# Performance work log

Measured on AMD Instinct MI355X. Metric: run time of the kernel, lower is better.

The kernel has to match this reference:

```python
import jax, jax.numpy as jnp
import numpy as np

HEADS = 8


def setup_inputs() -> dict:
    key = jax.random.key(0)
    ks = jax.random.split(key, 5)
    B, C, H, W = 2, 256, 48, 48
    s = 0.02
    return {
        "ct": jax.random.normal(ks[0], (B, C, H, W), jnp.float32),
        "us": jax.random.normal(ks[1], (B, C, H, W), jnp.float32),
        "w_qkv_ct": jax.random.normal(ks[2], (3 * C, C), jnp.float32) * s,
        "w_qkv_us": jax.random.normal(ks[3], (3 * C, C), jnp.float32) * s,
        "w_proj": jax.random.normal(ks[4], (C, 2 * C), jnp.float32) * s,
        "b_proj": jnp.zeros((C,), jnp.float32),
    }


def _heads_view(x, B, H, W):
    # [B, C, H, W] -> [B, heads, HW, dh]
    C = x.shape[1]
    return x.reshape(B, HEADS, C // HEADS, H * W).transpose(0, 1, 3, 2)


def _cross_attn(q, k, v, scale):
    # q,k,v: [B, heads, HW, dh]
    attn = jax.nn.softmax(jnp.einsum("bhnd,bhmd->bhnm", q, k) * scale, axis=-1)
    return jnp.einsum("bhnm,bhmd->bhnd", attn, v)


def reference(ct, us, w_qkv_ct, w_qkv_us, w_proj, b_proj):
    B, C, H, W = ct.shape
    dh = C // HEADS
    scale = dh ** (-0.5)

    # 1x1 convs as channel GEMMs
    qkv1 = jnp.einsum("oc,bchw->bohw", w_qkv_ct, ct)
    qkv2 = jnp.einsum("oc,bchw->bohw", w_qkv_us, us)
    q1, k1, v1 = jnp.split(qkv1, 3, axis=1)
    q2, k2, v2 = jnp.split(qkv2, 3, axis=1)

    # CT queries attend to US keys/values
    o1 = _cross_attn(_heads_view(q1, B, H, W), _heads_view(k2, B, H, W),
                     _heads_view(v2, B, H, W), scale)
    # US queries attend to CT keys/values
    o2 = _cross_attn(_heads_view(q2, B, H, W), _heads_view(k1, B, H, W),
                     _heads_view(v1, B, H, W), scale)

    # [B, heads, HW, dh] -> [B, C, H, W]
    out1 = o1.transpose(0, 1, 3, 2).reshape(B, C, H, W)
    out2 = o2.transpose(0, 1, 3, 2).reshape(B, C, H, W)

    fused = jnp.concatenate([ct + out1, us + out2], axis=1)
    return jnp.einsum("oc,bchw->bohw", w_proj, fused) + b_proj[None, :, None, None]
```

## Files before the change

### kernel.cpp

```cpp
#include <hip/hip_runtime.h>
#include <hip/hip_bf16.h>
#include <math.h>

#define HW   2304
#define CCH  256

#define QSCALE 0.25504368686637270f

typedef short short8 __attribute__((ext_vector_type(8)));
typedef float f32x4  __attribute__((ext_vector_type(4)));

__device__ inline unsigned short f2bf(float f) {
    union { float f; unsigned u; } v; v.f = f;
    unsigned r = v.u + 0x7FFF + ((v.u >> 16) & 1);
    return (unsigned short)(r >> 16);
}
__device__ inline unsigned pkbf2(float a, float b) {
    float2 f; f.x = a; f.y = b;
    union { __hip_bfloat162 h; unsigned u; } c;
    c.h = __float22bfloat162_rn(f);
    return c.u;
}
__device__ inline unsigned pktrunc(float a, float b) {
    return __builtin_amdgcn_perm(__builtin_bit_cast(unsigned, b),
                                 __builtin_bit_cast(unsigned, a), 0x07060302u);
}


__device__ __forceinline__ void prep_unit(
    int u, int t,
    const float* __restrict__ ct, const float* __restrict__ us,
    const float* __restrict__ w1, const float* __restrict__ w2,
    const float* __restrict__ w3,
    unsigned short* __restrict__ xT,
    unsigned short* __restrict__ wb1, unsigned short* __restrict__ wb2,
    unsigned short* __restrict__ w3b,
    unsigned short* __restrict__ Ts )
{
    if (u >= 576) {
        const int v_ = u - 576;
        int z, base;
        if (v_ < 192)      { z = 0; base = v_ * 1024; }
        else if (v_ < 384) { z = 1; base = (v_ - 192) * 1024; }
        else               { z = 2; base = (v_ - 384) * 1024; }
        const float* s = (z == 0) ? w1 : (z == 1) ? w2 : w3;
        unsigned short* d = (z == 0) ? wb1 : (z == 1) ? wb2 : w3b;
        const int i = base + t * 4;
        const float4 v4 = *(const float4*)&s[i];
        const float sc = (z < 2 && i < 65536) ? QSCALE : 1.f;
        uint2 p; p.x = pkbf2(v4.x * sc, v4.y * sc); p.y = pkbf2(v4.z * sc, v4.w * sc);
        *(uint2*)&d[i] = p;
        return;
    }
    const int pt = u % 36, rest = u / 36, ctile = rest & 3, z = rest >> 2;
    const float* __restrict__ src = ((z >> 1) ? us : ct) + (size_t)(z & 1) * CCH * HW;
    unsigned short* __restrict__ dst = xT + (size_t)z * HW * 256;
    const int p0 = pt * 64, c0 = ctile * 64;
    const int m = t & 15, ms = (m & 7) << 3;
    __syncthreads();
#pragma unroll
    for (int r = 0; r < 4; r++) {
        const int c = (t >> 4) + 16 * r;
        const float4 v4 = *(const float4*)&src[(size_t)(c0 + c) * HW + p0 + m * 4];
        const int cs = c ^ ms;
        Ts[(m * 4 + 0) * 72 + cs] = f2bf(v4.x);
        Ts[(m * 4 + 1) * 72 + cs] = f2bf(v4.y);
        Ts[(m * 4 + 2) * 72 + cs] = f2bf(v4.z);
        Ts[(m * 4 + 3) * 72 + cs] = f2bf(v4.w);
    }
    __syncthreads();
    const int p = t >> 2, c8 = (t & 3) * 16;
    const int es = ((p >> 2) & 7) << 3;
    const short8 a  = *(const short8*)&Ts[p * 72 + (c8 ^ es)];
    const short8 b8 = *(const short8*)&Ts[p * 72 + ((c8 + 8) ^ es)];
    *(short8*)&dst[(size_t)(p0 + p) * 256 + c0 + c8]     = a;
    *(short8*)&dst[(size_t)(p0 + p) * 256 + c0 + c8 + 8] = b8;
}

__device__ __forceinline__ void qkv_unit(
    int ptile, int otile, int z, int t,
    const unsigned short* __restrict__ xT,
    const unsigned short* __restrict__ wb1, const unsigned short* __restrict__ wb2,
    unsigned short* __restrict__ qkvT1, unsigned short* __restrict__ qkvT2,
    unsigned short* __restrict__ vdm1,  unsigned short* __restrict__ vdm2,
    unsigned short* __restrict__ Ws, unsigned short* __restrict__ Xs)
{
    const int inp = z >> 1, b = z & 1;
    const unsigned short* __restrict__ X = xT + (size_t)(inp * 2 + b) * HW * 256;
    const unsigned short* __restrict__ W = inp ? wb2 : wb1;
    unsigned short* __restrict__ qT = (inp ? qkvT2 : qkvT1) + (size_t)b * HW * 512;
    unsigned short* __restrict__ vd = (inp ? vdm2 : vdm1) + (size_t)b * CCH * HW;
    const int p0 = ptile * 64, o0 = otile * 64;
    const int w = t >> 6, lane = t & 63, quad = lane >> 4, m = lane & 15;
    const int sr = t >> 3, sc = t & 7;

    f32x4 acc[4] = {{0,0,0,0},{0,0,0,0},{0,0,0,0},{0,0,0,0}};

    short8 wv0 = *(const short8*)&W[(size_t)(o0 + sr) * 256 + sc * 8];
    short8 wv1 = *(const short8*)&W[(size_t)(o0 + 32 + sr) * 256 + sc * 8];
    short8 xv0 = *(const short8*)&X[(size_t)(p0 + sr) * 256 + sc * 8];
    short8 xv1 = *(const short8*)&X[(size_t)(p0 + 32 + sr) * 256 + sc * 8];

    for (int k0 = 0; k0 < 256; k0 += 64) {
        __syncthreads();
        *(short8*)&Ws[sr * 72 + sc * 8] = wv0;
        *(short8*)&Ws[(32 + sr) * 72 + sc * 8] = wv1;
        *(short8*)&Xs[sr * 72 + sc * 8] = xv0;
        *(short8*)&Xs[(32 + sr) * 72 + sc * 8] = xv1;
        __syncthreads();
        const int kn = k0 + 64;
        if (kn < 256) {
            wv0 = *(const short8*)&W[(size_t)(o0 + sr) * 256 + kn + sc * 8];
            wv1 = *(const short8*)&W[(size_t)(o0 + 32 + sr) * 256 + kn + sc * 8];
            xv0 = *(const short8*)&X[(size_t)(p0 + sr) * 256 + kn + sc * 8];
            xv1 = *(const short8*)&X[(size_t)(p0 + 32 + sr) * 256 + kn + sc * 8];
        }
#pragma unroll
        for (int kc2 = 0; kc2 < 2; kc2++) {
            const short8 af = *(const short8*)&Ws[(w * 16 + m) * 72 + kc2 * 32 + quad * 8];
#pragma unroll
            for (int pg = 0; pg < 4; pg++) {
                const short8 bf = *(const short8*)&Xs[(pg * 16 + m) * 72 + kc2 * 32 + quad * 8];
                acc[pg] = __builtin_amdgcn_mfma_f32_16x16x32_bf16(af, bf, acc[pg], 0, 0, 0);
            }
        }
    }
    __syncthreads();
    if (o0 < 512) {
#pragma unroll
        for (int pg = 0; pg < 4; pg++) {
            uint2 pk; pk.x = pkbf2(acc[pg][0], acc[pg][1]); pk.y = pkbf2(acc[pg][2], acc[pg][3]);
            *(uint2*)&Ws[(pg * 16 + m) * 72 + w * 16 + quad * 4] = pk;
        }
        __syncthreads();
        const int pr = t >> 2, cc = t & 3;
        const uint4 d0 = *(const uint4*)&Ws[pr * 72 + cc * 16];
        const uint4 d1 = *(const uint4*)&Ws[pr * 72 + cc * 16 + 8];
        *(uint4*)&qT[(size_t)(p0 + pr) * 512 + o0 + cc * 16]     = d0;
        *(uint4*)&qT[(size_t)(p0 + pr) * 512 + o0 + cc * 16 + 8] = d1;
    } else {
#pragma unroll
        for (int pg = 0; pg < 4; pg++)
#pragma unroll
            for (int r = 0; r < 4; r++)
                Ws[(w * 16 + quad * 4 + r) * 72 + pg * 16 + m] = f2bf(acc[pg][r]);
        __syncthreads();
        const int dr = t >> 2, cc = t & 3;
        const uint4 d0 = *(const uint4*)&Ws[dr * 72 + cc * 16];
        const uint4 d1 = *(const uint4*)&Ws[dr * 72 + cc * 16 + 8];
        *(uint4*)&vd[(size_t)(o0 - 512 + dr) * HW + p0 + cc * 16]     = d0;
        *(uint4*)&vd[(size_t)(o0 - 512 + dr) * HW + p0 + cc * 16 + 8] = d1;
    }
    __syncthreads();
}

__device__ __forceinline__ void attn_unit(
    int ptile, int dir, int b, int h, int t,
    const unsigned short* __restrict__ qkvT1, const unsigned short* __restrict__ qkvT2,
    const unsigned short* __restrict__ vdm1,  const unsigned short* __restrict__ vdm2,
    const float* __restrict__ ct, const float* __restrict__ us,
    unsigned short* __restrict__ fusedT,
    unsigned short* __restrict__ Ks , unsigned short* __restrict__ Vs )
{
    const unsigned short* __restrict__ Qt = (dir ? qkvT2 : qkvT1) + (size_t)b * HW * 512;
    const unsigned short* __restrict__ Kt = (dir ? qkvT1 : qkvT2) + (size_t)b * HW * 512
                                            + 256 + h * 32;
    const unsigned short* __restrict__ Vd = (dir ? vdm1 : vdm2) + ((size_t)b * CCH + h * 32) * HW;
    const float* __restrict__ src = (dir ? us : ct) + ((size_t)b * CCH + h * 32) * HW;

    const int w = t >> 6, lane = t & 63, quad = lane >> 4, m = lane & 15;
    const int kj0 = t >> 2, kcs = t & 3;
    const int pcK = kcs ^ (((kj0 >> 1) & 1) | (((kj0 >> 3) & 1) << 1));
    const int vr0 = t >> 4, vcs = t & 15;
    const int g2m = ((m >> 1) & 1) | (((m >> 2) & 1) << 1);
    const unsigned short* __restrict__ ksb =
        &Ks[((m >> 2) * 8 + (m & 3)) * 32 + (quad ^ g2m) * 8];
    const unsigned short* __restrict__ vsb = &Vs[m * 136 + quad * 8];
    const short ONE = (short)0x3F80;
    const short8 ones = {ONE,ONE,ONE,ONE,ONE,ONE,ONE,ONE};

    const int pqA = ptile * 128 + w * 32 + m;
    const short8 qfA = *(const short8*)&Qt[(size_t)pqA * 512 + h * 32 + quad * 8];
    const short8 qfB = *(const short8*)&Qt[(size_t)(pqA + 16) * 512 + h * 32 + quad * 8];

    f32x4 acc0A = {0,0,0,0}, acc1A = {0,0,0,0}, acclA = {0,0,0,0};
    f32x4 acc0B = {0,0,0,0}, acc1B = {0,0,0,0}, acclB = {0,0,0,0};

    short8 ka = *(const short8*)&Kt[(size_t)kj0 * 512 + kcs * 8];
    short8 kb = *(const short8*)&Kt[(size_t)(kj0 + 64) * 512 + kcs * 8];
    short8 va = *(const short8*)&Vd[(size_t)vr0 * HW + vcs * 8];
    short8 vb = *(const short8*)&Vd[(size_t)(vr0 + 16) * HW + vcs * 8];

    for (int j0 = 0; j0 < HW; j0 += 128) {
        __syncthreads();
        *(short8*)&Ks[kj0 * 32 + pcK * 8] = ka;
        *(short8*)&Ks[(kj0 + 64) * 32 + pcK * 8] = kb;
        *(short8*)&Vs[vr0 * 136 + vcs * 8] = va;
        *(short8*)&Vs[(vr0 + 16) * 136 + vcs * 8] = vb;
        __syncthreads();

        const int jn = j0 + 128;
        if (jn < HW) {
            ka = *(const short8*)&Kt[(size_t)(jn + kj0) * 512 + kcs * 8];
            kb = *(const short8*)&Kt[(size_t)(jn + kj0 + 64) * 512 + kcs * 8];
            va = *(const short8*)&Vd[(size_t)vr0 * HW + jn + vcs * 8];
            vb = *(const short8*)&Vd[(size_t)(vr0 + 16) * HW + jn + vcs * 8];
        }

        uint4 pwA[4], pwB[4];
#pragma unroll
        for (int f = 0; f < 8; f++) {
            const short8 kf = *(const short8*)(ksb + ((f >> 1) * 32 + (f & 1) * 4) * 32);
            const f32x4 z = {0,0,0,0};
            const f32x4 SA = __builtin_amdgcn_mfma_f32_16x16x32_bf16(kf, qfA, z, 0, 0, 0);
            const f32x4 SB = __builtin_amdgcn_mfma_f32_16x16x32_bf16(kf, qfB, z, 0, 0, 0);
            const float a0 = __builtin_amdgcn_exp2f(SA[0]);
            const float a1 = __builtin_amdgcn_exp2f(SA[1]);
            const float a2 = __builtin_amdgcn_exp2f(SA[2]);
            const float a3 = __builtin_amdgcn_exp2f(SA[3]);
            const float b0 = __builtin_amdgcn_exp2f(SB[0]);
            const float b1 = __builtin_amdgcn_exp2f(SB[1]);
            const float b2 = __builtin_amdgcn_exp2f(SB[2]);
            const float b3 = __builtin_amdgcn_exp2f(SB[3]);
            if ((f & 1) == 0) {
                pwA[f >> 1].x = pktrunc(a0, a1); pwA[f >> 1].y = pktrunc(a2, a3);
                pwB[f >> 1].x = pktrunc(b0, b1); pwB[f >> 1].y = pktrunc(b2, b3);
            } else {
                pwA[f >> 1].z = pktrunc(a0, a1); pwA[f >> 1].w = pktrunc(a2, a3);
                pwB[f >> 1].z = pktrunc(b0, b1); pwB[f >> 1].w = pktrunc(b2, b3);
            }
        }
#pragma unroll
        for (int kt = 0; kt < 4; kt++) {
            const short8 pfA = __builtin_bit_cast(short8, pwA[kt]);
            const short8 pfB = __builtin_bit_cast(short8, pwB[kt]);
            const short8 vf0 = *(const short8*)(vsb + kt * 32);
            const short8 vf1 = *(const short8*)(vsb + 16 * 136 + kt * 32);
            acc0A = __builtin_amdgcn_mfma_f32_16x16x32_bf16(vf0, pfA, acc0A, 0, 0, 0);
            acc1A = __builtin_amdgcn_mfma_f32_16x16x32_bf16(vf1, pfA, acc1A, 0, 0, 0);
            acclA = __builtin_amdgcn_mfma_f32_16x16x32_bf16(ones, pfA, acclA, 0, 0, 0);
            acc0B = __builtin_amdgcn_mfma_f32_16x16x32_bf16(vf0, pfB, acc0B, 0, 0, 0);
            acc1B = __builtin_amdgcn_mfma_f32_16x16x32_bf16(vf1, pfB, acc1B, 0, 0, 0);
            acclB = __builtin_amdgcn_mfma_f32_16x16x32_bf16(ones, pfB, acclB, 0, 0, 0);
        }
    }

    const int cb = dir * 256 + h * 32, d0 = quad * 4;
    {
        const float inv = 1.f / acclA[0];
        unsigned short* __restrict__ fT = fusedT + ((size_t)b * HW + pqA) * 512 + cb + d0;
        uint2 s0, s1;
        s0.x = pkbf2(acc0A[0] * inv + src[(size_t)(d0 + 0) * HW + pqA],
                     acc0A[1] * inv + src[(size_t)(d0 + 1) * HW + pqA]);
        s0.y = pkbf2(acc0A[2] * inv + src[(size_t)(d0 + 2) * HW + pqA],
                     acc0A[3] * inv + src[(size_t)(d0 + 3) * HW + pqA]);
        s1.x = pkbf2(acc1A[0] * inv + src[(size_t)(16 + d0 + 0) * HW + pqA],
                     acc1A[1] * inv + src[(size_t)(16 + d0 + 1) * HW + pqA]);
        s1.y = pkbf2(acc1A[2] * inv + src[(size_t)(16 + d0 + 2) * HW + pqA],
                     acc1A[3] * inv + src[(size_t)(16 + d0 + 3) * HW + pqA]);
        *(uint2*)&fT[0]  = s0;
        *(uint2*)&fT[16] = s1;
    }
    {
        const int pqB = pqA + 16;
        const float inv = 1.f / acclB[0];
        unsigned short* __restrict__ fT = fusedT + ((size_t)b * HW + pqB) * 512 + cb + d0;
        uint2 s0, s1;
        s0.x = pkbf2(acc0B[0] * inv + src[(size_t)(d0 + 0) * HW + pqB],
                     acc0B[1] * inv + src[(size_t)(d0 + 1) * HW + pqB]);
        s0.y = pkbf2(acc0B[2] * inv + src[(size_t)(d0 + 2) * HW + pqB],
                     acc0B[3] * inv + src[(size_t)(d0 + 3) * HW + pqB]);
        s1.x = pkbf2(acc1B[0] * inv + src[(size_t)(16 + d0 + 0) * HW + pqB],
                     acc1B[1] * inv + src[(size_t)(16 + d0 + 1) * HW + pqB]);
        s1.y = pkbf2(acc1B[2] * inv + src[(size_t)(16 + d0 + 2) * HW + pqB],
                     acc1B[3] * inv + src[(size_t)(16 + d0 + 3) * HW + pqB]);
        *(uint2*)&fT[0]  = s0;
        *(uint2*)&fT[16] = s1;
    }
    __syncthreads();
}

__device__ __forceinline__ void proj_unit(
    int ptile, int otile, int t,
    const unsigned short* __restrict__ w3b, const unsigned short* __restrict__ fusedT,
    const float* __restrict__ bias, float* __restrict__ out,
    unsigned short* __restrict__ Ws, unsigned short* __restrict__ Xs)
{
    const int p0 = ptile * 64, o0 = otile * 64;
    const int w = t >> 6, lane = t & 63, quad = lane >> 4, m = lane & 15;
    const int sr = t >> 3, sc = t & 7;

    f32x4 acc[4] = {{0,0,0,0},{0,0,0,0},{0,0,0,0},{0,0,0,0}};

    short8 wv0 = *(const short8*)&w3b[(size_t)(o0 + sr) * 512 + sc * 8];
    short8 wv1 = *(const short8*)&w3b[(size_t)(o0 + 32 + sr) * 512 + sc * 8];
    short8 xv0 = *(const short8*)&fusedT[(size_t)(p0 + sr) * 512 + sc * 8];
    short8 xv1 = *(const short8*)&fusedT[(size_t)(p0 + 32 + sr) * 512 + sc * 8];

    for (int k0 = 0; k0 < 512; k0 += 64) {
        __syncthreads();
        *(short8*)&Ws[sr * 72 + sc * 8] = wv0;
        *(short8*)&Ws[(32 + sr) * 72 + sc * 8] = wv1;
        *(short8*)&Xs[sr * 72 + sc * 8] = xv0;
        *(short8*)&Xs[(32 + sr) * 72 + sc * 8] = xv1;
        __syncthreads();
        const int kn = k0 + 64;
        if (kn < 512) {
            wv0 = *(const short8*)&w3b[(size_t)(o0 + sr) * 512 + kn + sc * 8];
            wv1 = *(const short8*)&w3b[(size_t)(o0 + 32 + sr) * 512 + kn + sc * 8];
            xv0 = *(const short8*)&fusedT[(size_t)(p0 + sr) * 512 + kn + sc * 8];
            xv1 = *(const short8*)&fusedT[(size_t)(p0 + 32 + sr) * 512 + kn + sc * 8];
        }
#pragma unroll
        for (int kc2 = 0; kc2 < 2; kc2++) {
            const short8 af = *(const short8*)&Ws[(w * 16 + m) * 72 + kc2 * 32 + quad * 8];
#pragma unroll
            for (int pg = 0; pg < 4; pg++) {
                const short8 bf = *(const short8*)&Xs[(pg * 16 + m) * 72 + kc2 * 32 + quad * 8];
                acc[pg] = __builtin_amdgcn_mfma_f32_16x16x32_bf16(af, bf, acc[pg], 0, 0, 0);
            }
        }
    }
    const int b = (p0 >= HW) ? 1 : 0;
    const int pl0 = p0 - b * HW;
    float* __restrict__ ob = out + (size_t)b * CCH * HW;
    float b4[4];
#pragma unroll
    for (int r = 0; r < 4; r++) b4[r] = bias[o0 + w * 16 + quad * 4 + r];
#pragma unroll
    for (int pg = 0; pg < 4; pg++)
#pragma unroll
        for (int r = 0; r < 4; r++)
            ob[(size_t)(o0 + w * 16 + quad * 4 + r) * HW + pl0 + pg * 16 + m]
                = acc[pg][r] + b4[r];
}

__global__ __launch_bounds__(256, 4) void prep_k(
    const float* __restrict__ ct, const float* __restrict__ us,
    const float* __restrict__ w1, const float* __restrict__ w2,
    const float* __restrict__ w3,
    unsigned short* __restrict__ xT,
    unsigned short* __restrict__ b1, unsigned short* __restrict__ b2,
    unsigned short* __restrict__ b3)
{
    __shared__ __align__(16) unsigned short Ts[64 * 72];
    prep_unit(blockIdx.x, threadIdx.x, ct, us, w1, w2, w3, xT, b1, b2, b3, Ts);
}

__global__ __launch_bounds__(256, 4) void qkv_k(
    const unsigned short* __restrict__ xT,
    const unsigned short* __restrict__ wb1, const unsigned short* __restrict__ wb2,
    unsigned short* __restrict__ qkvT1, unsigned short* __restrict__ qkvT2,
    unsigned short* __restrict__ vdm1,  unsigned short* __restrict__ vdm2)
{
    __shared__ __align__(16) unsigned short Ws[64 * 72];
    __shared__ __align__(16) unsigned short Xs[64 * 72];
    qkv_unit(blockIdx.x, blockIdx.y, blockIdx.z, threadIdx.x,
             xT, wb1, wb2, qkvT1, qkvT2, vdm1, vdm2, Ws, Xs);
}

__global__ __launch_bounds__(256, 3) void attn_k(
    const unsigned short* __restrict__ qkvT1, const unsigned short* __restrict__ qkvT2,
    const unsigned short* __restrict__ vdm1,  const unsigned short* __restrict__ vdm2,
    const float* __restrict__ ct, const float* __restrict__ us,
    unsigned short* __restrict__ fusedT)
{
    __shared__ __align__(16) unsigned short Ks[128 * 32];
    __shared__ __align__(16) unsigned short Vs[32 * 136];
    attn_unit(blockIdx.x, blockIdx.z, blockIdx.y >> 3, blockIdx.y & 7, threadIdx.x,
              qkvT1, qkvT2, vdm1, vdm2, ct, us, fusedT, Ks, Vs);
}

__global__ __launch_bounds__(256, 4) void proj_k(
    const unsigned short* __restrict__ w3b, const unsigned short* __restrict__ fusedT,
    const float* __restrict__ bias, float* __restrict__ out)
{
    __shared__ __align__(16) unsigned short Ws[64 * 72];
    __shared__ __align__(16) unsigned short Xs[64 * 72];
    proj_unit(blockIdx.x, blockIdx.y, threadIdx.x, w3b, fusedT, bias, out, Ws, Xs);
}

extern "C" void kernel_launch(void* const* d_in, const int* in_sizes, int n_in,
                              void* d_out, int out_size, void* d_ws, size_t ws_size,
                              hipStream_t stream)
{
    const float* ct       = (const float*)d_in[0];
    const float* us       = (const float*)d_in[1];
    const float* w_qkv_ct = (const float*)d_in[2];
    const float* w_qkv_us = (const float*)d_in[3];
    const float* w_proj   = (const float*)d_in[4];
    const float* b_proj   = (const float*)d_in[5];
    float* out = (float*)d_out;

    unsigned short* wb1   = (unsigned short*)d_ws;
    unsigned short* wb2   = wb1 + (size_t)768 * 256;
    unsigned short* w3b   = wb2 + (size_t)768 * 256;
    unsigned short* xT    = w3b + (size_t)256 * 512;
    unsigned short* qkvT1 = xT    + (size_t)4 * HW * 256;
    unsigned short* qkvT2 = qkvT1 + (size_t)2 * HW * 512;
    unsigned short* vdm1  = qkvT2 + (size_t)2 * HW * 512;
    unsigned short* vdm2  = vdm1  + (size_t)2 * CCH * HW;
    unsigned short* fusedT= vdm2  + (size_t)2 * CCH * HW;

    prep_k<<<dim3(1088), 256, 0, stream>>>(ct, us, w_qkv_ct, w_qkv_us, w_proj,
                                           xT, wb1, wb2, w3b);
    qkv_k <<<dim3(36, 12, 4), 256, 0, stream>>>(xT, wb1, wb2, qkvT1, qkvT2, vdm1, vdm2);
    attn_k<<<dim3(18, 16, 2), 256, 0, stream>>>(qkvT1, qkvT2, vdm1, vdm2, ct, us, fusedT);
    proj_k<<<dim3(72, 4), 256, 0, stream>>>(w3b, fusedT, b_proj, out);
}
```

Baseline: 125.4 us.

## Keep full X tile resident in LDS and loop over three output tiles per block

Result: slower. 128.0 us (+2.0%).

```diff
diff --git a/kernel.cpp b/kernel.cpp
--- a/kernel.cpp
+++ b/kernel.cpp
@@ -56,7 +56,7 @@
     const float* __restrict__ src = ((z >> 1) ? us : ct) + (size_t)(z & 1) * CCH * HW;
     unsigned short* __restrict__ dst = xT + (size_t)z * HW * 256;
     const int p0 = pt * 64, c0 = ctile * 64;
-    const int m = t & 15, ms = (m & 7) << 3;
+    const int m = t & 15, ms = ((m >> 1) & 7) << 3;
     __syncthreads();
 #pragma unroll
     for (int r = 0; r < 4; r++) {
@@ -70,7 +70,7 @@
     }
     __syncthreads();
     const int p = t >> 2, c8 = (t & 3) * 16;
-    const int es = ((p >> 2) & 7) << 3;
+    const int es = ((p >> 3) & 7) << 3;
     const short8 a  = *(const short8*)&Ts[p * 72 + (c8 ^ es)];
     const short8 b8 = *(const short8*)&Ts[p * 72 + ((c8 + 8) ^ es)];
     *(short8*)&dst[(size_t)(p0 + p) * 256 + c0 + c8]     = a;
@@ -78,80 +78,93 @@
 }
 
 __device__ __forceinline__ void qkv_unit(
-    int ptile, int otile, int z, int t,
+    int ptile, int og, int z, int t,
     const unsigned short* __restrict__ xT,
     const unsigned short* __restrict__ wb1, const unsigned short* __restrict__ wb2,
     unsigned short* __restrict__ qkvT1, unsigned short* __restrict__ qkvT2,
     unsigned short* __restrict__ vdm1,  unsigned short* __restrict__ vdm2,
-    unsigned short* __restrict__ Ws, unsigned short* __restrict__ Xs)
+    unsigned short* __restrict__ Ws , unsigned short* __restrict__ Xs )
 {
     const int inp = z >> 1, b = z & 1;
     const unsigned short* __restrict__ X = xT + (size_t)(inp * 2 + b) * HW * 256;
     const unsigned short* __restrict__ W = inp ? wb2 : wb1;
     unsigned short* __restrict__ qT = (inp ? qkvT2 : qkvT1) + (size_t)b * HW * 512;
     unsigned short* __restrict__ vd = (inp ? vdm2 : vdm1) + (size_t)b * CCH * HW;
-    const int p0 = ptile * 64, o0 = otile * 64;
+    const int p0 = ptile * 64, ob = og * 192;
     const int w = t >> 6, lane = t & 63, quad = lane >> 4, m = lane & 15;
     const int sr = t >> 3, sc = t & 7;
 
-    f32x4 acc[4] = {{0,0,0,0},{0,0,0,0},{0,0,0,0},{0,0,0,0}};
-
-    short8 wv0 = *(const short8*)&W[(size_t)(o0 + sr) * 256 + sc * 8];
-    short8 wv1 = *(const short8*)&W[(size_t)(o0 + 32 + sr) * 256 + sc * 8];
-    short8 xv0 = *(const short8*)&X[(size_t)(p0 + sr) * 256 + sc * 8];
-    short8 xv1 = *(const short8*)&X[(size_t)(p0 + 32 + sr) * 256 + sc * 8];
-
-    for (int k0 = 0; k0 < 256; k0 += 64) {
+    {
+        const int xr = t >> 3, xc = t & 7;
+#pragma unroll
+        for (int hh = 0; hh < 2; hh++)
+#pragma unroll
+            for (int i = 0; i < 4; i++)
+                *(short8*)&Xs[(size_t)(xr + 32 * hh) * 264 + xc * 8 + 64 * i] =
+                    *(const short8*)&X[(size_t)(p0 + xr + 32 * hh) * 256 + xc * 8 + 64 * i];
+    }
+
+    short8 wv0 = *(const short8*)&W[(size_t)(ob + sr) * 256 + sc * 8];
+    short8 wv1 = *(const short8*)&W[(size_t)(ob + 32 + sr) * 256 + sc * 8];
+
+    f32x4 acc[4];
+    for (int s = 0; s < 12; s++) {
+        const int ot = s >> 2, k0 = (s & 3) << 6;
+        const int o0 = ob + ot * 64;
+        if ((s & 3) == 0) {
+#pragma unroll
+            for (int pg = 0; pg < 4; pg++) acc[pg] = (f32x4){0, 0, 0, 0};
+        }
         __syncthreads();
         *(short8*)&Ws[sr * 72 + sc * 8] = wv0;
         *(short8*)&Ws[(32 + sr) * 72 + sc * 8] = wv1;
-        *(short8*)&Xs[sr * 72 + sc * 8] = xv0;
-        *(short8*)&Xs[(32 + sr) * 72 + sc * 8] = xv1;
-        __syncthreads();
-        const int kn = k0 + 64;
-        if (kn < 256) {
-            wv0 = *(const short8*)&W[(size_t)(o0 + sr) * 256 + kn + sc * 8];
-            wv1 = *(const short8*)&W[(size_t)(o0 + 32 + sr) * 256 + kn + sc * 8];
-            xv0 = *(const short8*)&X[(size_t)(p0 + sr) * 256 + kn + sc * 8];
-            xv1 = *(const short8*)&X[(size_t)(p0 + 32 + sr) * 256 + kn + sc * 8];
+        __syncthreads();
+        if (s < 11) {
+            const int sn = s + 1;
+            const int on = ob + (sn >> 2) * 64, kn = (sn & 3) << 6;
+            wv0 = *(const short8*)&W[(size_t)(on + sr) * 256 + kn + sc * 8];
+            wv1 = *(const short8*)&W[(size_t)(on + 32 + sr) * 256 + kn + sc * 8];
         }
 #pragma unroll
         for (int kc2 = 0; kc2 < 2; kc2++) {
             const short8 af = *(const short8*)&Ws[(w * 16 + m) * 72 + kc2 * 32 + quad * 8];
 #pragma unroll
             for (int pg = 0; pg < 4; pg++) {
-                const short8 bf = *(const short8*)&Xs[(pg * 16 + m) * 72 + kc2 * 32 + quad * 8];
+                const short8 bf = *(const short8*)&Xs[(size_t)(pg * 16 + m) * 264
+                                                      + k0 + kc2 * 32 + quad * 8];
                 acc[pg] = __builtin_amdgcn_mfma_f32_16x16x32_bf16(af, bf, acc[pg], 0, 0, 0);
             }
         }
-    }
-    __syncthreads();
-    if (o0 < 512) {
-#pragma unroll
-        for (int pg = 0; pg < 4; pg++) {
-            uint2 pk; pk.x = pkbf2(acc[pg][0], acc[pg][1]); pk.y = pkbf2(acc[pg][2], acc[pg][3]);
-            *(uint2*)&Ws[(pg * 16 + m) * 72 + w * 16 + quad * 4] = pk;
-        }
-        __syncthreads();
-        const int pr = t >> 2, cc = t & 3;
-        const uint4 d0 = *(const uint4*)&Ws[pr * 72 + cc * 16];
-        const uint4 d1 = *(const uint4*)&Ws[pr * 72 + cc * 16 + 8];
-        *(uint4*)&qT[(size_t)(p0 + pr) * 512 + o0 + cc * 16]     = d0;
-        *(uint4*)&qT[(size_t)(p0 + pr) * 512 + o0 + cc * 16 + 8] = d1;
-    } else {
-#pragma unroll
-        for (int pg = 0; pg < 4; pg++)
-#pragma unroll
-            for (int r = 0; r < 4; r++)
-                Ws[(w * 16 + quad * 4 + r) * 72 + pg * 16 + m] = f2bf(acc[pg][r]);
-        __syncthreads();
-        const int dr = t >> 2, cc = t & 3;
-        const uint4 d0 = *(const uint4*)&Ws[dr * 72 + cc * 16];
-        const uint4 d1 = *(const uint4*)&Ws[dr * 72 + cc * 16 + 8];
-        *(uint4*)&vd[(size_t)(o0 - 512 + dr) * HW + p0 + cc * 16]     = d0;
-        *(uint4*)&vd[(size_t)(o0 - 512 + dr) * HW + p0 + cc * 16 + 8] = d1;
-    }
-    __syncthreads();
+        if ((s & 3) == 3) {
+            __syncthreads();
+            if (o0 < 512) {
+#pragma unroll
+                for (int pg = 0; pg < 4; pg++) {
+                    uint2 pk; pk.x = pkbf2(acc[pg][0], acc[pg][1]);
+                    pk.y = pkbf2(acc[pg][2], acc[pg][3]);
+                    *(uint2*)&Ws[(pg * 16 + m) * 72 + w * 16 + quad * 4] = pk;
+                }
+                __syncthreads();
+                const int pr = t >> 2, cc = t & 3;
+                const uint4 d0 = *(const uint4*)&Ws[pr * 72 + cc * 16];
+                const uint4 d1 = *(const uint4*)&Ws[pr * 72 + cc * 16 + 8];
+                *(uint4*)&qT[(size_t)(p0 + pr) * 512 + o0 + cc * 16]     = d0;
+                *(uint4*)&qT[(size_t)(p0 + pr) * 512 + o0 + cc * 16 + 8] = d1;
+            } else {
+#pragma unroll
+                for (int pg = 0; pg < 4; pg++)
+#pragma unroll
+                    for (int r = 0; r < 4; r++)
+                        Ws[(w * 16 + quad * 4 + r) * 72 + pg * 16 + m] = f2bf(acc[pg][r]);
+                __syncthreads();
+                const int dr = t >> 2, cc = t & 3;
+                const uint4 d0 = *(const uint4*)&Ws[dr * 72 + cc * 16];
+                const uint4 d1 = *(const uint4*)&Ws[dr * 72 + cc * 16 + 8];
+                *(uint4*)&vd[(size_t)(o0 - 512 + dr) * HW + p0 + cc * 16]     = d0;
+                *(uint4*)&vd[(size_t)(o0 - 512 + dr) * HW + p0 + cc * 16 + 8] = d1;
+            }
+        }
+    }
 }
 
 __device__ __forceinline__ void attn_unit(
@@ -347,14 +360,14 @@
     prep_unit(blockIdx.x, threadIdx.x, ct, us, w1, w2, w3, xT, b1, b2, b3, Ts);
 }
 
-__global__ __launch_bounds__(256, 4) void qkv_k(
+__global__ __launch_bounds__(256, 3) void qkv_k(
     const unsigned short* __restrict__ xT,
     const unsigned short* __restrict__ wb1, const unsigned short* __restrict__ wb2,
     unsigned short* __restrict__ qkvT1, unsigned short* __restrict__ qkvT2,
     unsigned short* __restrict__ vdm1,  unsigned short* __restrict__ vdm2)
 {
     __shared__ __align__(16) unsigned short Ws[64 * 72];
-    __shared__ __align__(16) unsigned short Xs[64 * 72];
+    __shared__ __align__(16) unsigned short Xs[64 * 264];
     qkv_unit(blockIdx.x, blockIdx.y, blockIdx.z, threadIdx.x,
              xT, wb1, wb2, qkvT1, qkvT2, vdm1, vdm2, Ws, Xs);
 }
@@ -404,7 +417,7 @@
 
     prep_k<<<dim3(1088), 256, 0, stream>>>(ct, us, w_qkv_ct, w_qkv_us, w_proj,
                                            xT, wb1, wb2, w3b);
-    qkv_k <<<dim3(36, 12, 4), 256, 0, stream>>>(xT, wb1, wb2, qkvT1, qkvT2, vdm1, vdm2);
+    qkv_k <<<dim3(36, 4, 4), 256, 0, stream>>>(xT, wb1, wb2, qkvT1, qkvT2, vdm1, vdm2);
     attn_k<<<dim3(18, 16, 2), 256, 0, stream>>>(qkvT1, qkvT2, vdm1, vdm2, ct, us, fusedT);
     proj_k<<<dim3(72, 4), 256, 0, stream>>>(w3b, fusedT, b_proj, out);
 }
```

## Split attention key range across two thread groups with LDS reduction

Applied to the files above, without the earlier changes.

Result: slower. 144.4 us (+15.1%).

```diff
diff --git a/kernel.cpp b/kernel.cpp
--- a/kernel.cpp
+++ b/kernel.cpp
@@ -56,7 +56,7 @@
     const float* __restrict__ src = ((z >> 1) ? us : ct) + (size_t)(z & 1) * CCH * HW;
     unsigned short* __restrict__ dst = xT + (size_t)z * HW * 256;
     const int p0 = pt * 64, c0 = ctile * 64;
-    const int m = t & 15, ms = (m & 7) << 3;
+    const int m = t & 15, ms = ((m >> 1) & 7) << 3;
     __syncthreads();
 #pragma unroll
     for (int r = 0; r < 4; r++) {
@@ -70,7 +70,7 @@
     }
     __syncthreads();
     const int p = t >> 2, c8 = (t & 3) * 16;
-    const int es = ((p >> 2) & 7) << 3;
+    const int es = ((p >> 3) & 7) << 3;
     const short8 a  = *(const short8*)&Ts[p * 72 + (c8 ^ es)];
     const short8 b8 = *(const short8*)&Ts[p * 72 + ((c8 + 8) ^ es)];
     *(short8*)&dst[(size_t)(p0 + p) * 256 + c0 + c8]     = a;
@@ -154,24 +154,110 @@
     __syncthreads();
 }
 
-__device__ __forceinline__ void attn_unit(
-    int ptile, int dir, int b, int h, int t,
+__device__ __forceinline__ void proj_unit(
+    int ptile, int otile, int t,
+    const unsigned short* __restrict__ w3b, const unsigned short* __restrict__ fusedT,
+    const float* __restrict__ bias, float* __restrict__ out,
+    unsigned short* __restrict__ Ws, unsigned short* __restrict__ Xs)
+{
+    const int p0 = ptile * 64, o0 = otile * 64;
+    const int w = t >> 6, lane = t & 63, quad = lane >> 4, m = lane & 15;
+    const int sr = t >> 3, sc = t & 7;
+
+    f32x4 acc[4] = {{0,0,0,0},{0,0,0,0},{0,0,0,0},{0,0,0,0}};
+
+    short8 wv0 = *(const short8*)&w3b[(size_t)(o0 + sr) * 512 + sc * 8];
+    short8 wv1 = *(const short8*)&w3b[(size_t)(o0 + 32 + sr) * 512 + sc * 8];
+    short8 xv0 = *(const short8*)&fusedT[(size_t)(p0 + sr) * 512 + sc * 8];
+    short8 xv1 = *(const short8*)&fusedT[(size_t)(p0 + 32 + sr) * 512 + sc * 8];
+
+    for (int k0 = 0; k0 < 512; k0 += 64) {
+        __syncthreads();
+        *(short8*)&Ws[sr * 72 + sc * 8] = wv0;
+        *(short8*)&Ws[(32 + sr) * 72 + sc * 8] = wv1;
+        *(short8*)&Xs[sr * 72 + sc * 8] = xv0;
+        *(short8*)&Xs[(32 + sr) * 72 + sc * 8] = xv1;
+        __syncthreads();
+        const int kn = k0 + 64;
+        if (kn < 512) {
+            wv0 = *(const short8*)&w3b[(size_t)(o0 + sr) * 512 + kn + sc * 8];
+            wv1 = *(const short8*)&w3b[(size_t)(o0 + 32 + sr) * 512 + kn + sc * 8];
+            xv0 = *(const short8*)&fusedT[(size_t)(p0 + sr) * 512 + kn + sc * 8];
+            xv1 = *(const short8*)&fusedT[(size_t)(p0 + 32 + sr) * 512 + kn + sc * 8];
+        }
+#pragma unroll
+        for (int kc2 = 0; kc2 < 2; kc2++) {
+            const short8 af = *(const short8*)&Ws[(w * 16 + m) * 72 + kc2 * 32 + quad * 8];
+#pragma unroll
+            for (int pg = 0; pg < 4; pg++) {
+                const short8 bf = *(const short8*)&Xs[(pg * 16 + m) * 72 + kc2 * 32 + quad * 8];
+                acc[pg] = __builtin_amdgcn_mfma_f32_16x16x32_bf16(af, bf, acc[pg], 0, 0, 0);
+            }
+        }
+    }
+    const int b = (p0 >= HW) ? 1 : 0;
+    const int pl0 = p0 - b * HW;
+    float* __restrict__ ob = out + (size_t)b * CCH * HW;
+    float b4[4];
+#pragma unroll
+    for (int r = 0; r < 4; r++) b4[r] = bias[o0 + w * 16 + quad * 4 + r];
+#pragma unroll
+    for (int pg = 0; pg < 4; pg++)
+#pragma unroll
+        for (int r = 0; r < 4; r++)
+            ob[(size_t)(o0 + w * 16 + quad * 4 + r) * HW + pl0 + pg * 16 + m]
+                = acc[pg][r] + b4[r];
+}
+
+__global__ __launch_bounds__(256, 4) void prep_k(
+    const float* __restrict__ ct, const float* __restrict__ us,
+    const float* __restrict__ w1, const float* __restrict__ w2,
+    const float* __restrict__ w3,
+    unsigned short* __restrict__ xT,
+    unsigned short* __restrict__ b1, unsigned short* __restrict__ b2,
+    unsigned short* __restrict__ b3)
+{
+    __shared__ __align__(16) unsigned short Ts[64 * 72];
+    prep_unit(blockIdx.x, threadIdx.x, ct, us, w1, w2, w3, xT, b1, b2, b3, Ts);
+}
+
+__global__ __launch_bounds__(256, 4) void qkv_k(
+    const unsigned short* __restrict__ xT,
+    const unsigned short* __restrict__ wb1, const unsigned short* __restrict__ wb2,
+    unsigned short* __restrict__ qkvT1, unsigned short* __restrict__ qkvT2,
+    unsigned short* __restrict__ vdm1,  unsigned short* __restrict__ vdm2)
+{
+    __shared__ __align__(16) unsigned short Ws[64 * 72];
+    __shared__ __align__(16) unsigned short Xs[64 * 72];
+    qkv_unit(blockIdx.x, blockIdx.y, blockIdx.z, threadIdx.x,
+             xT, wb1, wb2, qkvT1, qkvT2, vdm1, vdm2, Ws, Xs);
+}
+
+__global__ __launch_bounds__(512, 6) void attn_k(
     const unsigned short* __restrict__ qkvT1, const unsigned short* __restrict__ qkvT2,
     const unsigned short* __restrict__ vdm1,  const unsigned short* __restrict__ vdm2,
     const float* __restrict__ ct, const float* __restrict__ us,
-    unsigned short* __restrict__ fusedT,
-    unsigned short* __restrict__ Ks , unsigned short* __restrict__ Vs )
-{
+    unsigned short* __restrict__ fusedT)
+{
+    __shared__ __align__(16) unsigned short smem[16896];
+    const int t = threadIdx.x;
+    const int g = t >> 8, tl = t & 255;
+    unsigned short* __restrict__ Ks = smem + g * 8448;
+    unsigned short* __restrict__ Vs = smem + g * 8448 + 4096;
+
+    const int ptile = blockIdx.x, dir = blockIdx.z;
+    const int b = blockIdx.y >> 3, h = blockIdx.y & 7;
+
     const unsigned short* __restrict__ Qt = (dir ? qkvT2 : qkvT1) + (size_t)b * HW * 512;
     const unsigned short* __restrict__ Kt = (dir ? qkvT1 : qkvT2) + (size_t)b * HW * 512
                                             + 256 + h * 32;
     const unsigned short* __restrict__ Vd = (dir ? vdm1 : vdm2) + ((size_t)b * CCH + h * 32) * HW;
     const float* __restrict__ src = (dir ? us : ct) + ((size_t)b * CCH + h * 32) * HW;
 
-    const int w = t >> 6, lane = t & 63, quad = lane >> 4, m = lane & 15;
-    const int kj0 = t >> 2, kcs = t & 3;
+    const int w = tl >> 6, lane = tl & 63, quad = lane >> 4, m = lane & 15;
+    const int kj0 = tl >> 2, kcs = tl & 3;
     const int pcK = kcs ^ (((kj0 >> 1) & 1) | (((kj0 >> 3) & 1) << 1));
-    const int vr0 = t >> 4, vcs = t & 15;
+    const int vr0 = tl >> 4, vcs = tl & 15;
     const int g2m = ((m >> 1) & 1) | (((m >> 2) & 1) << 1);
     const unsigned short* __restrict__ ksb =
         &Ks[((m >> 2) * 8 + (m & 3)) * 32 + (quad ^ g2m) * 8];
@@ -179,6 +265,7 @@
     const short ONE = (short)0x3F80;
     const short8 ones = {ONE,ONE,ONE,ONE,ONE,ONE,ONE,ONE};
 
+    const int jb = g * 1152;
     const int pqA = ptile * 128 + w * 32 + m;
     const short8 qfA = *(const short8*)&Qt[(size_t)pqA * 512 + h * 32 + quad * 8];
     const short8 qfB = *(const short8*)&Qt[(size_t)(pqA + 16) * 512 + h * 32 + quad * 8];
@@ -186,12 +273,12 @@
     f32x4 acc0A = {0,0,0,0}, acc1A = {0,0,0,0}, acclA = {0,0,0,0};
     f32x4 acc0B = {0,0,0,0}, acc1B = {0,0,0,0}, acclB = {0,0,0,0};
 
-    short8 ka = *(const short8*)&Kt[(size_t)kj0 * 512 + kcs * 8];
-    short8 kb = *(const short8*)&Kt[(size_t)(kj0 + 64) * 512 + kcs * 8];
-    short8 va = *(const short8*)&Vd[(size_t)vr0 * HW + vcs * 8];
-    short8 vb = *(const short8*)&Vd[(size_t)(vr0 + 16) * HW + vcs * 8];
-
-    for (int j0 = 0; j0 < HW; j0 += 128) {
+    short8 ka = *(const short8*)&Kt[(size_t)(jb + kj0) * 512 + kcs * 8];
+    short8 kb = *(const short8*)&Kt[(size_t)(jb + kj0 + 64) * 512 + kcs * 8];
+    short8 va = *(const short8*)&Vd[(size_t)vr0 * HW + jb + vcs * 8];
+    short8 vb = *(const short8*)&Vd[(size_t)(vr0 + 16) * HW + jb + vcs * 8];
+
+    for (int j0 = 0; j0 < 1152; j0 += 128) {
         __syncthreads();
         *(short8*)&Ks[kj0 * 32 + pcK * 8] = ka;
         *(short8*)&Ks[(kj0 + 64) * 32 + pcK * 8] = kb;
@@ -200,11 +287,11 @@
         __syncthreads();
 
         const int jn = j0 + 128;
-        if (jn < HW) {
-            ka = *(const short8*)&Kt[(size_t)(jn + kj0) * 512 + kcs * 8];
-            kb = *(const short8*)&Kt[(size_t)(jn + kj0 + 64) * 512 + kcs * 8];
-            va = *(const short8*)&Vd[(size_t)vr0 * HW + jn + vcs * 8];
-            vb = *(const short8*)&Vd[(size_t)(vr0 + 16) * HW + jn + vcs * 8];
+        if (jn < 1152) {
+            ka = *(const short8*)&Kt[(size_t)(jb + jn + kj0) * 512 + kcs * 8];
+            kb = *(const short8*)&Kt[(size_t)(jb + jn + kj0 + 64) * 512 + kcs * 8];
+            va = *(const short8*)&Vd[(size_t)vr0 * HW + jb + jn + vcs * 8];
+            vb = *(const short8*)&Vd[(size_t)(vr0 + 16) * HW + jb + jn + vcs * 8];
         }
 
         uint4 pwA[4], pwB[4];
@@ -245,130 +332,59 @@
         }
     }
 
-    const int cb = dir * 256 + h * 32, d0 = quad * 4;
-    {
-        const float inv = 1.f / acclA[0];
-        unsigned short* __restrict__ fT = fusedT + ((size_t)b * HW + pqA) * 512 + cb + d0;
-        uint2 s0, s1;
-        s0.x = pkbf2(acc0A[0] * inv + src[(size_t)(d0 + 0) * HW + pqA],
-                     acc0A[1] * inv + src[(size_t)(d0 + 1) * HW + pqA]);
-        s0.y = pkbf2(acc0A[2] * inv + src[(size_t)(d0 + 2) * HW + pqA],
-                     acc0A[3] * inv + src[(size_t)(d0 + 3) * HW + pqA]);
-        s1.x = pkbf2(acc1A[0] * inv + src[(size_t)(16 + d0 + 0) * HW + pqA],
-                     acc1A[1] * inv + src[(size_t)(16 + d0 + 1) * HW + pqA]);
-        s1.y = pkbf2(acc1A[2] * inv + src[(size_t)(16 + d0 + 2) * HW + pqA],
-                     acc1A[3] * inv + src[(size_t)(16 + d0 + 3) * HW + pqA]);
-        *(uint2*)&fT[0]  = s0;
-        *(uint2*)&fT[16] = s1;
-    }
-    {
-        const int pqB = pqA + 16;
-        const float inv = 1.f / acclB[0];
-        unsigned short* __restrict__ fT = fusedT + ((size_t)b * HW + pqB) * 512 + cb + d0;
-        uint2 s0, s1;
-        s0.x = pkbf2(acc0B[0] * inv + src[(size_t)(d0 + 0) * HW + pqB],
-                     acc0B[1] * inv + src[(size_t)(d0 + 1) * HW + pqB]);
-        s0.y = pkbf2(acc0B[2] * inv + src[(size_t)(d0 + 2) * HW + pqB],
-                     acc0B[3] * inv + src[(size_t)(d0 + 3) * HW + pqB]);
-        s1.x = pkbf2(acc1B[0] * inv + src[(size_t)(16 + d0 + 0) * HW + pqB],
-                     acc1B[1] * inv + src[(size_t)(16 + d0 + 1) * HW + pqB]);
-        s1.y = pkbf2(acc1B[2] * inv + src[(size_t)(16 + d0 + 2) * HW + pqB],
-                     acc1B[3] * inv + src[(size_t)(16 + d0 + 3) * HW + pqB]);
-        *(uint2*)&fT[0]  = s0;
-        *(uint2*)&fT[16] = s1;
-    }
-    __syncthreads();
-}
-
-__device__ __forceinline__ void proj_unit(
-    int ptile, int otile, int t,
-    const unsigned short* __restrict__ w3b, const unsigned short* __restrict__ fusedT,
-    const float* __restrict__ bias, float* __restrict__ out,
-    unsigned short* __restrict__ Ws, unsigned short* __restrict__ Xs)
-{
-    const int p0 = ptile * 64, o0 = otile * 64;
-    const int w = t >> 6, lane = t & 63, quad = lane >> 4, m = lane & 15;
-    const int sr = t >> 3, sc = t & 7;
-
-    f32x4 acc[4] = {{0,0,0,0},{0,0,0,0},{0,0,0,0},{0,0,0,0}};
-
-    short8 wv0 = *(const short8*)&w3b[(size_t)(o0 + sr) * 512 + sc * 8];
-    short8 wv1 = *(const short8*)&w3b[(size_t)(o0 + 32 + sr) * 512 + sc * 8];
-    short8 xv0 = *(const short8*)&fusedT[(size_t)(p0 + sr) * 512 + sc * 8];
-    short8 xv1 = *(const short8*)&fusedT[(size_t)(p0 + 32 + sr) * 512 + sc * 8];
-
-    for (int k0 = 0; k0 < 512; k0 += 64) {
-        __syncthreads();
-        *(short8*)&Ws[sr * 72 + sc * 8] = wv0;
-        *(short8*)&Ws[(32 + sr) * 72 + sc * 8] = wv1;
-        *(short8*)&Xs[sr * 72 + sc * 8] = xv0;
-        *(short8*)&Xs[(32 + sr) * 72 + sc * 8] = xv1;
-        __syncthreads();
-        const int kn = k0 + 64;
-        if (kn < 512) {
-            wv0 = *(const short8*)&w3b[(size_t)(o0 + sr) * 512 + kn + sc * 8];
-            wv1 = *(const short8*)&w3b[(size_t)(o0 + 32 + sr) * 512 + kn + sc * 8];
-            xv0 = *(const short8*)&fusedT[(size_t)(p0 + sr) * 512 + kn + sc * 8];
-            xv1 = *(const short8*)&fusedT[(size_t)(p0 + 32 + sr) * 512 + kn + sc * 8];
-        }
-#pragma unroll
-        for (int kc2 = 0; kc2 < 2; kc2++) {
-            const short8 af = *(const short8*)&Ws[(w * 16 + m) * 72 + kc2 * 32 + quad * 8];
-#pragma unroll
-            for (int pg = 0; pg < 4; pg++) {
-                const short8 bf = *(const short8*)&Xs[(pg * 16 + m) * 72 + kc2 * 32 + quad * 8];
-                acc[pg] = __builtin_amdgcn_mfma_f32_16x16x32_bf16(af, bf, acc[pg], 0, 0, 0);
-            }
-        }
-    }
-    const int b = (p0 >= HW) ? 1 : 0;
-    const int pl0 = p0 - b * HW;
-    float* __restrict__ ob = out + (size_t)b * CCH * HW;
-    float b4[4];
-#pragma unroll
-    for (int r = 0; r < 4; r++) b4[r] = bias[o0 + w * 16 + quad * 4 + r];
-#pragma unroll
-    for (int pg = 0; pg < 4; pg++)
-#pragma unroll
-        for (int r = 0; r < 4; r++)
-            ob[(size_t)(o0 + w * 16 + quad * 4 + r) * HW + pl0 + pg * 16 + m]
-                = acc[pg][r] + b4[r];
-}
-
-__global__ __launch_bounds__(256, 4) void prep_k(
-    const float* __restrict__ ct, const float* __restrict__ us,
-    const float* __restrict__ w1, const float* __restrict__ w2,
-    const float* __restrict__ w3,
-    unsigned short* __restrict__ xT,
-    unsigned short* __restrict__ b1, unsigned short* __restrict__ b2,
-    unsigned short* __restrict__ b3)
-{
-    __shared__ __align__(16) unsigned short Ts[64 * 72];
-    prep_unit(blockIdx.x, threadIdx.x, ct, us, w1, w2, w3, xT, b1, b2, b3, Ts);
-}
-
-__global__ __launch_bounds__(256, 4) void qkv_k(
-    const unsigned short* __restrict__ xT,
-    const unsigned short* __restrict__ wb1, const unsigned short* __restrict__ wb2,
-    unsigned short* __restrict__ qkvT1, unsigned short* __restrict__ qkvT2,
-    unsigned short* __restrict__ vdm1,  unsigned short* __restrict__ vdm2)
-{
-    __shared__ __align__(16) unsigned short Ws[64 * 72];
-    __shared__ __align__(16) unsigned short Xs[64 * 72];
-    qkv_unit(blockIdx.x, blockIdx.y, blockIdx.z, threadIdx.x,
-             xT, wb1, wb2, qkvT1, qkvT2, vdm1, vdm2, Ws, Xs);
-}
-
-__global__ __launch_bounds__(256, 3) void attn_k(
-    const unsigned short* __restrict__ qkvT1, const unsigned short* __restrict__ qkvT2,
-    const unsigned short* __restrict__ vdm1,  const unsigned short* __restrict__ vdm2,
-    const float* __restrict__ ct, const float* __restrict__ us,
-    unsigned short* __restrict__ fusedT)
-{
-    __shared__ __align__(16) unsigned short Ks[128 * 32];
-    __shared__ __align__(16) unsigned short Vs[32 * 136];
-    attn_unit(blockIdx.x, blockIdx.z, blockIdx.y >> 3, blockIdx.y & 7, threadIdx.x,
-              qkvT1, qkvT2, vdm1, vdm2, ct, us, fusedT, Ks, Vs);
+    __syncthreads();
+    float* __restrict__ cbuf = (float*)smem;
+    const int slot = (w * 64 + lane) * 20;
+    if (g == 1) {
+        *(f32x4*)&cbuf[slot + 0]  = acc0A;
+        *(f32x4*)&cbuf[slot + 4]  = acc1A;
+        *(f32x4*)&cbuf[slot + 8]  = acc0B;
+        *(f32x4*)&cbuf[slot + 12] = acc1B;
+        cbuf[slot + 16] = acclA[0];
+        cbuf[slot + 17] = acclB[0];
+    }
+    __syncthreads();
+    if (g == 0) {
+        acc0A += *(const f32x4*)&cbuf[slot + 0];
+        acc1A += *(const f32x4*)&cbuf[slot + 4];
+        acc0B += *(const f32x4*)&cbuf[slot + 8];
+        acc1B += *(const f32x4*)&cbuf[slot + 12];
+        const float lA = acclA[0] + cbuf[slot + 16];
+        const float lB = acclB[0] + cbuf[slot + 17];
+
+        const int cb = dir * 256 + h * 32, d0 = quad * 4;
+        {
+            const float inv = 1.f / lA;
+            unsigned short* __restrict__ fT = fusedT + ((size_t)b * HW + pqA) * 512 + cb + d0;
+            uint2 s0, s1;
+            s0.x = pkbf2(acc0A[0] * inv + src[(size_t)(d0 + 0) * HW + pqA],
+                         acc0A[1] * inv + src[(size_t)(d0 + 1) * HW + pqA]);
+            s0.y = pkbf2(acc0A[2] * inv + src[(size_t)(d0 + 2) * HW + pqA],
+                         acc0A[3] * inv + src[(size_t)(d0 + 3) * HW + pqA]);
+            s1.x = pkbf2(acc1A[0] * inv + src[(size_t)(16 + d0 + 0) * HW + pqA],
+                         acc1A[1] * inv + src[(size_t)(16 + d0 + 1) * HW + pqA]);
+            s1.y = pkbf2(acc1A[2] * inv + src[(size_t)(16 + d0 + 2) * HW + pqA],
+                         acc1A[3] * inv + src[(size_t)(16 + d0 + 3) * HW + pqA]);
+            *(uint2*)&fT[0]  = s0;
+            *(uint2*)&fT[16] = s1;
+        }
+        {
+            const int pqB = pqA + 16;
+            const float inv = 1.f / lB;
+            unsigned short* __restrict__ fT = fusedT + ((size_t)b * HW + pqB) * 512 + cb + d0;
+            uint2 s0, s1;
+            s0.x = pkbf2(acc0B[0] * inv + src[(size_t)(d0 + 0) * HW + pqB],
+                         acc0B[1] * inv + src[(size_t)(d0 + 1) * HW + pqB]);
+            s0.y = pkbf2(acc0B[2] * inv + src[(size_t)(d0 + 2) * HW + pqB],
+                         acc0B[3] * inv + src[(size_t)(d0 + 3) * HW + pqB]);
+            s1.x = pkbf2(acc1B[0] * inv + src[(size_t)(16 + d0 + 0) * HW + pqB],
+                         acc1B[1] * inv + src[(size_t)(16 + d0 + 1) * HW + pqB]);
+            s1.y = pkbf2(acc1B[2] * inv + src[(size_t)(16 + d0 + 2) * HW + pqB],
+                         acc1B[3] * inv + src[(size_t)(16 + d0 + 3) * HW + pqB]);
+            *(uint2*)&fT[0]  = s0;
+            *(uint2*)&fT[16] = s1;
+        }
+    }
 }
 
 __global__ __launch_bounds__(256, 4) void proj_k(
@@ -405,6 +421,6 @@
     prep_k<<<dim3(1088), 256, 0, stream>>>(ct, us, w_qkv_ct, w_qkv_us, w_proj,
                                            xT, wb1, wb2, w3b);
     qkv_k <<<dim3(36, 12, 4), 256, 0, stream>>>(xT, wb1, wb2, qkvT1, qkvT2, vdm1, vdm2);
-    attn_k<<<dim3(18, 16, 2), 256, 0, stream>>>(qkvT1, qkvT2, vdm1, vdm2, ct, us, fusedT);
+    attn_k<<<dim3(18, 16, 2), 512, 0, stream>>>(qkvT1, qkvT2, vdm1, vdm2, ct, us, fusedT);
     proj_k<<<dim3(72, 4), 256, 0, stream>>>(w3b, fusedT, b_proj, out);
 }
```
